# Kernel tuning notes

Measured on AMD Instinct MI355X. Metric: run time of the kernel, lower is better.

The kernel has to match this reference:

```python
import jax, jax.numpy as jnp
import numpy as np

B, S = 4, 1024
H = 32
NOPE, ROPE, VDIM = 128, 64, 128
Q_LORA, KV_LORA = 1536, 512
SCALE = 1.0 / np.sqrt(NOPE + ROPE)


def _make_rope(total, d, dtype=jnp.float32):
    # gen_rope: theta_j = 10000^{-2j/d}, idx = pos * theta, tiled x2 -> (T,1,d)
    theta = 1.0 / (10000.0 ** (jnp.arange(0, d, 2, dtype=dtype) / d))
    idx = jnp.arange(total, dtype=dtype)[:, None] * theta[None, :]  # (T, d/2)
    idx = jnp.tile(idx, (1, 2))[:, None, :]                          # (T, 1, d)
    return jnp.cos(idx), jnp.sin(idx)


def _apply_rope(x, cos, sin):
    # x: (T, heads, d); cos/sin: (T, 1, d). Matches torch apply_rope:
    # deinterleave even/odd then rotate-half.
    d = x.shape[-1]
    xp = jnp.concatenate([x[..., 0::2], x[..., 1::2]], axis=-1)
    rot = jnp.concatenate([-xp[..., d // 2:], xp[..., : d // 2]], axis=-1)
    return xp * cos + rot * sin


def setup_inputs() -> dict:
    key = jax.random.key(0)
    ks = jax.random.split(key, 5)
    Q = jax.random.normal(ks[0], (B, S, Q_LORA), dtype=jnp.float32)
    KV = jax.random.normal(ks[1], (B, S, KV_LORA), dtype=jnp.float32)
    PE = jax.random.normal(ks[2], (B, S, ROPE), dtype=jnp.float32)
    WUQ = jax.random.normal(ks[3], (H * (NOPE + ROPE), Q_LORA), dtype=jnp.float32) / np.sqrt(Q_LORA)
    WUKV = jax.random.normal(ks[4], (H * (NOPE + VDIM), KV_LORA), dtype=jnp.float32) / np.sqrt(KV_LORA)
    cos, sin = _make_rope(B * S, ROPE)
    return {"Q": Q, "KV": KV, "PE": PE, "WUQ": WUQ, "WUKV": WUKV, "cos": cos, "sin": sin}


def reference(Q, KV, PE, WUQ, WUKV, cos, sin):
    # Up-project Q latent -> per-head (nope + rope) dims
    q = jnp.einsum('bsl,el->bse', Q, WUQ).reshape(B, S, H, NOPE + ROPE)
    q_nope, q_pe = q[..., :NOPE], q[..., NOPE:]
    q_pe = _apply_rope(q_pe.reshape(B * S, H, ROPE), cos, sin).reshape(B, S, H, ROPE)
    # Shared (per-token) rotary key part
    k_pe = _apply_rope(PE.reshape(B * S, 1, ROPE), cos, sin).reshape(B, S, 1, ROPE)
    # Up-project KV latent -> per-head (k_nope + v)
    kvu = jnp.einsum('bsl,el->bse', KV, WUKV).reshape(B, S, H, NOPE + VDIM)
    k_nope, v = kvu[..., :NOPE], kvu[..., NOPE:]
    q_full = jnp.concatenate([q_nope, q_pe], axis=-1)                      # (B,S,H,192)
    k_full = jnp.concatenate([k_nope, jnp.broadcast_to(k_pe, (B, S, H, ROPE))], axis=-1)
    scores = jnp.einsum('bqhd,bkhd->bhqk', q_full, k_full) * SCALE        # (B,H,S,S)
    causal = jnp.tril(jnp.ones((S, S), dtype=bool))
    scores = jnp.where(causal, scores, jnp.finfo(scores.dtype).min)
    attn = jax.nn.softmax(scores, axis=-1)
    out = jnp.einsum('bhqk,bkhd->bqhd', attn, v)                          # (B,S,H,VDIM)
    return out
```

## Files before the change

kernel.cpp:

```cpp
#include <hip/hip_runtime.h>
#include <hip/hip_bf16.h>


typedef __attribute__((ext_vector_type(8))) short s8v;
typedef __attribute__((ext_vector_type(4))) short s4v;
typedef __attribute__((ext_vector_type(4))) float f4v;

#define B_ 4
#define S_ 1024
#define H_ 32
#define SCALE_ 0.07216878364870322992f

__device__ __forceinline__ short f2bf(float f) {
  unsigned u = __builtin_bit_cast(unsigned, f);
  unsigned r = (u + 0x7FFFu + ((u >> 16) & 1u)) >> 16;
  return (short)(unsigned short)r;
}

__device__ __forceinline__ void gll16(const void* g, void* l) {
  __builtin_amdgcn_global_load_lds((const __attribute__((address_space(1))) void*)g,
                                   (__attribute__((address_space(3))) void*)l, 16, 0, 0);
}

__global__ __launch_bounds__(256) void prep_kernel(
    const float* __restrict__ Q, const float* __restrict__ WUQ,
    const float* __restrict__ KV, const float* __restrict__ WUKV,
    const float* __restrict__ PE, const float* __restrict__ cosb,
    const float* __restrict__ sinb,
    short* __restrict__ Qb, short* __restrict__ Wq,
    short* __restrict__ KVb, short* __restrict__ Wkv,
    short* __restrict__ kfull) {
  const int b = blockIdx.x;
  if (b < 21504) {
    int i = b * 256 + threadIdx.x;
    const float* src; short* dst;
    if (i < 1572864)      { src = Q;    dst = Qb; }
    else if (i < 3932160) { src = WUQ;  dst = Wq;  i -= 1572864; }
    else if (i < 4456448) { src = KV;   dst = KVb; i -= 3932160; }
    else                  { src = WUKV; dst = Wkv; i -= 4456448; }
    float4 v = reinterpret_cast<const float4*>(src)[i];
    s4v o;
    o[0] = f2bf(v.x); o[1] = f2bf(v.y); o[2] = f2bf(v.z); o[3] = f2bf(v.w);
    reinterpret_cast<s4v*>(dst)[i] = o;
  } else {
    const int pos = (b - 21504) * 4 + (threadIdx.x >> 6);
    const int t = threadIdx.x & 63;
    const int p = t & 31;
    float x0 = PE[(size_t)pos * 64 + 2 * p];
    float x1 = PE[(size_t)pos * 64 + 2 * p + 1];
    float cv = cosb[(size_t)pos * 64 + p];
    float sv = sinb[(size_t)pos * 64 + p];
    float o = (t < 32) ? (x0 * cv - x1 * sv) : (x1 * cv + x0 * sv);
    short ob = f2bf(o);
    const int bb = pos >> 10, s = pos & 1023;
#pragma unroll
    for (int h = 0; h < H_; ++h)
      kfull[(((size_t)bb * H_ + h) * S_ + s) * 192 + 128 + t] = ob;
  }
}

template<int K, int MODE>
__device__ __forceinline__ void gemm_body(
    const int m0, const int n0, const short* __restrict__ A,
    const short* __restrict__ Bt, const float* __restrict__ cosb,
    const float* __restrict__ sinb, short* __restrict__ out0,
    short* __restrict__ out1, char* sAb, char* sBb) {
  const int tid = threadIdx.x;
  const int w = tid >> 6, l = tid & 63;
  const int l15 = l & 15, lg = l >> 4;
  const int wr = (w >> 1) * 64, wc = (w & 1) * 64;
  const int rs7 = l15 & 7;
  f4v acc[4][4] = {};
  const int srow = tid >> 3;
  const int swsl = (tid & 7) ^ (srow & 7);
  const char* gA = (const char*)A + ((size_t)(m0 + srow) * K + swsl * 8) * 2;
  const char* gB = (const char*)Bt + ((size_t)(n0 + srow) * K + swsl * 8) * 2;
  const int ldst = tid * 16;

#pragma unroll
  for (int r4 = 0; r4 < 4; ++r4) {
    gll16(gA + (size_t)r4 * (32 * K * 2), sAb + r4 * 4096 + ldst);
    gll16(gB + (size_t)r4 * (32 * K * 2), sBb + r4 * 4096 + ldst);
  }

  int cur = 0;
  for (int kk = 0; kk < K; kk += 64) {
    __syncthreads();
    if (kk + 64 < K) {
      const char* ga = gA + (size_t)(kk + 64) * 2;
      const char* gb = gB + (size_t)(kk + 64) * 2;
#pragma unroll
      for (int r4 = 0; r4 < 4; ++r4) {
        gll16(ga + (size_t)r4 * (32 * K * 2), sAb + (cur ^ 1) * 16384 + r4 * 4096 + ldst);
        gll16(gb + (size_t)r4 * (32 * K * 2), sBb + (cur ^ 1) * 16384 + r4 * 4096 + ldst);
      }
    }
#pragma unroll
    for (int kc = 0; kc < 2; ++kc) {
      s8v af[4], bfv[4];
#pragma unroll
      for (int x = 0; x < 4; ++x) {
        af[x]  = *(const s8v*)(sAb + cur * 16384 + (wr + x * 16 + l15) * 128 + (((kc * 4 + lg) ^ rs7) << 4));
        bfv[x] = *(const s8v*)(sBb + cur * 16384 + (wc + x * 16 + l15) * 128 + (((kc * 4 + lg) ^ rs7) << 4));
      }
#pragma unroll
      for (int i = 0; i < 4; ++i)
#pragma unroll
        for (int j = 0; j < 4; ++j)
          acc[i][j] = __builtin_amdgcn_mfma_f32_16x16x32_bf16(af[i], bfv[j], acc[i][j], 0, 0, 0);
    }
    cur ^= 1;
  }

#pragma unroll
  for (int j = 0; j < 4; ++j) {
    const int colb = n0 + wc + j * 16;
    if (MODE == 0) {
      const int e0 = colb % 192;
      const int h = colb / 192;
      const int e = e0 + l15;
      const bool is_pe = (e0 >= 128);
#pragma unroll
      for (int i = 0; i < 4; ++i) {
#pragma unroll
        for (int r = 0; r < 4; ++r) {
          const int row = m0 + wr + i * 16 + lg * 4 + r;
          const int b = row >> 10, s = row & 1023;
          const size_t base = ((size_t)(b * H_ + h) * S_ + s) * 192;
          float val = acc[i][j][r] * SCALE_;
          if (!is_pe) {
            out0[base + e] = f2bf(val);
          } else {
            float other = __shfl_xor(val, 1, 64);
            int p = (e - 128) >> 1;
            float cv = cosb[(size_t)row * 64 + p];
            float sv = sinb[(size_t)row * 64 + p];
            float o = ((l & 1) == 0) ? (val * cv - other * sv) : (val * cv + other * sv);
            int ep = ((l & 1) == 0) ? (128 + p) : (160 + p);
            out0[base + ep] = f2bf(o);
          }
        }
      }
    } else {
      const int e0 = colb % 256;
      const int h = colb / 256;
      const int e = e0 + l15;
      const bool is_v = (e0 >= 128);
#pragma unroll
      for (int i = 0; i < 4; ++i) {
#pragma unroll
        for (int r = 0; r < 4; ++r) {
          const int row = m0 + wr + i * 16 + lg * 4 + r;
          const int b = row >> 10, s = row & 1023;
          float val = acc[i][j][r];
          if (!is_v) {
            out0[((size_t)(b * H_ + h) * S_ + s) * 192 + e] = f2bf(val);
          } else {
            out1[((size_t)(b * H_ + h) * 128 + (e - 128)) * S_ + s] = f2bf(val);
          }
        }
      }
    }
  }
}

__global__ __launch_bounds__(256, 2) void gemm_fused(
    const short* __restrict__ Qb, const short* __restrict__ Wq,
    const short* __restrict__ KVb, const short* __restrict__ Wkv,
    const float* __restrict__ cosb, const float* __restrict__ sinb,
    short* __restrict__ qfull, short* __restrict__ kfull,
    short* __restrict__ vtb) {
  __shared__ char sAb[2 * 16384];
  __shared__ char sBb[2 * 16384];
  const int id = blockIdx.x;
  if (id < 1536) {
    const int xcd = id & 7, j = id >> 3;
    const int m0 = (xcd * 4 + (j & 3)) * 128;
    const int n0 = (j >> 2) * 128;
    gemm_body<1536, 0>(m0, n0, Qb, Wq, cosb, sinb, qfull, nullptr, sAb, sBb);
  } else {
    const int idp = id - 1536;
    const int xcd = idp & 7, j = idp >> 3;
    const int m0 = (xcd * 4 + (j & 3)) * 128;
    const int n0 = (j >> 2) * 128;
    gemm_body<512, 1>(m0, n0, KVb, Wkv, nullptr, nullptr, kfull, vtb, sAb, sBb);
  }
}

__global__ __launch_bounds__(256, 2) void attn_kernel(
    const short* __restrict__ qfull, const short* __restrict__ kfull,
    const short* __restrict__ vt, float* __restrict__ out) {
  __shared__ short sK[2][64 * 192];
  const int bid = blockIdx.x;
  const int qb = 7 - (bid >> 7);
  const int bh = bid & 127;
  const int b = bh >> 5, h = bh & 31;
  const int tid = threadIdx.x;
  const int w = tid >> 6, l = tid & 63;
  const int l15 = l & 15, lg = l >> 4;
  const short* Qh = qfull + (size_t)bh * (S_ * 192);
  const char*  KhB = (const char*)(kfull + (size_t)bh * (S_ * 192));
  const short* Vh = vt + (size_t)bh * (128 * S_);
  const int qw = qb * 128 + w * 32;

  s8v qfr[2][6];
#pragma unroll
  for (int mq = 0; mq < 2; ++mq)
#pragma unroll
    for (int kc = 0; kc < 6; ++kc)
      qfr[mq][kc] = *reinterpret_cast<const s8v*>(
          &Qh[(size_t)(qw + mq * 16 + l15) * 192 + kc * 32 + lg * 8]);

  unsigned kOff[6];
#pragma unroll
  for (int c = 0; c < 6; ++c) {
    unsigned o = (unsigned)(w * 6 + c) * 1024u + (unsigned)l * 16u;
    unsigned row = o / 384u;
    unsigned cb = o - row * 384u;
    kOff[c] = row * 384u + (cb ^ ((row & 7u) << 4));
  }

#pragma unroll
  for (int c = 0; c < 6; ++c)
    gll16(KhB + kOff[c], (char*)(&sK[0][0]) + (w * 6 + c) * 1024);
  __syncthreads();

  f4v acc[8][2] = {};
  float mrun[2] = {-3.0e38f, -3.0e38f};
  float lsum[2] = {0.f, 0.f};
  const int nt = 2 * (qb + 1);
  int cur = 0;
  for (int t = 0; t < nt; ++t) {
    const int k0 = t * 64;
    const bool compute = (k0 <= qw + 31);
    s8v vf0[8];
    if (compute) {
#pragma unroll
      for (int dt = 0; dt < 8; ++dt)
        vf0[dt] = *reinterpret_cast<const s8v*>(
            &Vh[(size_t)(dt * 16 + l15) * S_ + k0 + lg * 8]);
    }
    if (t + 1 < nt) {
      const char* gb = KhB + (size_t)(t + 1) * (64 * 384);
      char* lb = (char*)(&sK[cur ^ 1][0]);
#pragma unroll
      for (int c = 0; c < 6; ++c)
        gll16(gb + kOff[c], lb + (w * 6 + c) * 1024);
    }
    if (compute) {
      const char* sKc = (const char*)(&sK[cur][0]);
      f4v s[4][2] = {};
#pragma unroll
      for (int T = 0; T < 4; ++T) {
        const int row = T * 16 + l15;
        const unsigned swz = (unsigned)((row & 7) << 4);
#pragma unroll
        for (int kc = 0; kc < 6; ++kc) {
          s8v kf = *reinterpret_cast<const s8v*>(
              sKc + row * 384 + (unsigned)((kc * 64 + lg * 16) ^ swz));
          s[T][0] = __builtin_amdgcn_mfma_f32_16x16x32_bf16(kf, qfr[0][kc], s[T][0], 0, 0, 0);
          s[T][1] = __builtin_amdgcn_mfma_f32_16x16x32_bf16(kf, qfr[1][kc], s[T][1], 0, 0, 0);
        }
      }
      const bool diag = (t >= 2 * qb);
      unsigned pk[4][2][2];
#pragma unroll
      for (int mq = 0; mq < 2; ++mq) {
        const int qlane = qw + mq * 16 + l15;
        if (diag) {
#pragma unroll
          for (int T = 0; T < 4; ++T)
#pragma unroll
            for (int r = 0; r < 4; ++r)
              if (k0 + T * 16 + lg * 4 + r > qlane) s[T][mq][r] = -1.0e30f;
        }
        float tmax = s[0][mq][0];
#pragma unroll
        for (int T = 0; T < 4; ++T)
#pragma unroll
          for (int r = 0; r < 4; ++r) tmax = fmaxf(tmax, s[T][mq][r]);
        tmax = fmaxf(tmax, __shfl_xor(tmax, 16, 64));
        tmax = fmaxf(tmax, __shfl_xor(tmax, 32, 64));
        if (!__all(tmax <= mrun[mq] + 8.0f)) {
          const float mnew = fmaxf(mrun[mq], tmax);
          const float cf = __expf(mrun[mq] - mnew);
          mrun[mq] = mnew;
          lsum[mq] *= cf;
#pragma unroll
          for (int dt = 0; dt < 8; ++dt)
#pragma unroll
            for (int r = 0; r < 4; ++r) acc[dt][mq][r] *= cf;
        }
        float rs = 0.f;
#pragma unroll
        for (int T = 0; T < 4; ++T)
#pragma unroll
          for (int r = 0; r < 4; ++r) {
            float e = __expf(s[T][mq][r] - mrun[mq]);
            s[T][mq][r] = e;
            rs += e;
          }
        rs += __shfl_xor(rs, 16, 64);
        rs += __shfl_xor(rs, 32, 64);
        lsum[mq] += rs;
#pragma unroll
        for (int T = 0; T < 4; ++T) {
          pk[T][mq][0] = (unsigned)(unsigned short)f2bf(s[T][mq][0]) |
                         ((unsigned)(unsigned short)f2bf(s[T][mq][1]) << 16);
          pk[T][mq][1] = (unsigned)(unsigned short)f2bf(s[T][mq][2]) |
                         ((unsigned)(unsigned short)f2bf(s[T][mq][3]) << 16);
        }
      }
#pragma unroll
      for (int c2 = 0; c2 < 2; ++c2) {
        union { unsigned u[4]; s8v v; } bb[2];
#pragma unroll
        for (int mq = 0; mq < 2; ++mq)
#pragma unroll
          for (int j2 = 0; j2 < 4; ++j2) {
            int src = l15 + ((l & 16) << 1) + ((j2 & 2) << 3);
            unsigned va = (unsigned)__shfl((int)pk[2 * c2][mq][j2 & 1], src, 64);
            unsigned vb = (unsigned)__shfl((int)pk[2 * c2 + 1][mq][j2 & 1], src, 64);
            bb[mq].u[j2] = (l & 32) ? vb : va;
          }
#pragma unroll
        for (int dt = 0; dt < 8; ++dt) {
          s8v vfx = (c2 == 0) ? vf0[dt]
                              : *reinterpret_cast<const s8v*>(
                                    &Vh[(size_t)(dt * 16 + l15) * S_ + k0 + 32 + lg * 8]);
          acc[dt][0] = __builtin_amdgcn_mfma_f32_16x16x32_bf16(vfx, bb[0].v, acc[dt][0], 0, 0, 0);
          acc[dt][1] = __builtin_amdgcn_mfma_f32_16x16x32_bf16(vfx, bb[1].v, acc[dt][1], 0, 0, 0);
        }
      }
    }
    __syncthreads();
    cur ^= 1;
  }
#pragma unroll
  for (int mq = 0; mq < 2; ++mq) {
    const float inv = 1.0f / lsum[mq];
    const int q = qw + mq * 16 + l15;
    float* ob = out + (((size_t)b * S_ + q) * H_ + h) * 128 + lg * 4;
#pragma unroll
    for (int dt = 0; dt < 8; ++dt) {
      float4 o4 = { acc[dt][mq][0] * inv, acc[dt][mq][1] * inv,
                    acc[dt][mq][2] * inv, acc[dt][mq][3] * inv };
      *reinterpret_cast<float4*>(ob + dt * 16) = o4;
    }
  }
}

extern "C" void kernel_launch(void* const* d_in, const int* in_sizes, int n_in,
                              void* d_out, int out_size, void* d_ws, size_t ws_size,
                              hipStream_t stream) {
  const float* Q    = (const float*)d_in[0];
  const float* KV   = (const float*)d_in[1];
  const float* PE   = (const float*)d_in[2];
  const float* WUQ  = (const float*)d_in[3];
  const float* WUKV = (const float*)d_in[4];
  const float* cosb = (const float*)d_in[5];
  const float* sinb = (const float*)d_in[6];
  float* out = (float*)d_out;
  char* ws = (char*)d_ws;

  short* Qb    = (short*)(ws);
  short* Wq    = (short*)(ws + 12582912);
  short* KVb   = (short*)(ws + 31457280);
  short* Wkv   = (short*)(ws + 35651584);
  short* qfull = (short*)(ws + 44040192);
  short* kfull = (short*)(ws + 94371840);
  short* vtb   = (short*)(ws + 144703488);

  prep_kernel<<<22528, 256, 0, stream>>>(Q, WUQ, KV, WUKV, PE, cosb, sinb,
                                         Qb, Wq, KVb, Wkv, kfull);
  gemm_fused<<<3584, 256, 0, stream>>>(Qb, Wq, KVb, Wkv, cosb, sinb,
                                       qfull, kfull, vtb);
  attn_kernel<<<1024, 256, 0, stream>>>(qfull, kfull, vtb, out);
}
```

Before: 314.3 us.

## Enlarge GEMM tiles to 256x128 with 8 waves and triple-buffered LDS pipeline

Changes the fused up-projection GEMM from 128x128 tiles with 4 waves to 256x128 tiles with 8 waves and 512 threads, halving the grid. The previous double-buffered, sync-per-step loop becomes a three-stage global-to-LDS prefetch ring with explicit vmcnt waits and raw barriers. It also raises wave priority around the MFMA block and hoists B fragments out of the inner loop. The aim is to hide global load latency and improve operand reuse. The cost is a much larger LDS footprint (144KB), which likely allows only one block per CU despite the launch bound hint.

```diff
diff --git a/kernel.cpp b/kernel.cpp
--- a/kernel.cpp
+++ b/kernel.cpp
@@ -65,51 +65,67 @@
     const short* __restrict__ Bt, const float* __restrict__ cosb,
     const float* __restrict__ sinb, short* __restrict__ out0,
     short* __restrict__ out1, char* sAb, char* sBb) {
+  constexpr int NT = K / 64;
   const int tid = threadIdx.x;
   const int w = tid >> 6, l = tid & 63;
   const int l15 = l & 15, lg = l >> 4;
-  const int wr = (w >> 1) * 64, wc = (w & 1) * 64;
+  const int wr = (w >> 1) * 64;
+  const int wc = (w & 1) * 64;
   const int rs7 = l15 & 7;
   f4v acc[4][4] = {};
   const int srow = tid >> 3;
-  const int swsl = (tid & 7) ^ (srow & 7);
-  const char* gA = (const char*)A + ((size_t)(m0 + srow) * K + swsl * 8) * 2;
-  const char* gB = (const char*)Bt + ((size_t)(n0 + srow) * K + swsl * 8) * 2;
+  const int lslot = (tid & 7) ^ (srow & 7);
+  const char* gA = (const char*)A + ((size_t)(m0 + srow) * K + lslot * 8) * 2;
+  const char* gB = (const char*)Bt + ((size_t)(n0 + srow) * K + lslot * 8) * 2;
   const int ldst = tid * 16;
 
-#pragma unroll
-  for (int r4 = 0; r4 < 4; ++r4) {
-    gll16(gA + (size_t)r4 * (32 * K * 2), sAb + r4 * 4096 + ldst);
-    gll16(gB + (size_t)r4 * (32 * K * 2), sBb + r4 * 4096 + ldst);
-  }
-
-  int cur = 0;
-  for (int kk = 0; kk < K; kk += 64) {
-    __syncthreads();
-    if (kk + 64 < K) {
-      const char* ga = gA + (size_t)(kk + 64) * 2;
-      const char* gb = gB + (size_t)(kk + 64) * 2;
-#pragma unroll
-      for (int r4 = 0; r4 < 4; ++r4) {
-        gll16(ga + (size_t)r4 * (32 * K * 2), sAb + (cur ^ 1) * 16384 + r4 * 4096 + ldst);
-        gll16(gb + (size_t)r4 * (32 * K * 2), sBb + (cur ^ 1) * 16384 + r4 * 4096 + ldst);
-      }
-    }
-#pragma unroll
-    for (int kc = 0; kc < 2; ++kc) {
-      s8v af[4], bfv[4];
-#pragma unroll
-      for (int x = 0; x < 4; ++x) {
-        af[x]  = *(const s8v*)(sAb + cur * 16384 + (wr + x * 16 + l15) * 128 + (((kc * 4 + lg) ^ rs7) << 4));
-        bfv[x] = *(const s8v*)(sBb + cur * 16384 + (wc + x * 16 + l15) * 128 + (((kc * 4 + lg) ^ rs7) << 4));
-      }
-#pragma unroll
-      for (int i = 0; i < 4; ++i)
-#pragma unroll
-        for (int j = 0; j < 4; ++j)
-          acc[i][j] = __builtin_amdgcn_mfma_f32_16x16x32_bf16(af[i], bfv[j], acc[i][j], 0, 0, 0);
-    }
-    cur ^= 1;
+  auto stgA = [&](int buf, int kt) {
+#pragma unroll
+    for (int r4 = 0; r4 < 4; ++r4)
+      gll16(gA + (size_t)r4 * (64 * K * 2) + kt * 128, sAb + buf * 32768 + r4 * 8192 + ldst);
+  };
+  auto stgB = [&](int buf, int kt) {
+#pragma unroll
+    for (int r4 = 0; r4 < 2; ++r4)
+      gll16(gB + (size_t)r4 * (64 * K * 2) + kt * 128, sBb + buf * 16384 + r4 * 8192 + ldst);
+  };
+
+  stgA(0, 0); stgB(0, 0);
+  stgA(1, 1); stgB(1, 1);
+  asm volatile("s_waitcnt vmcnt(6)" ::: "memory");
+  __builtin_amdgcn_s_barrier();
+
+  int bi = 0;
+  for (int t = 0; t < NT; ++t) {
+    const char* bufA = sAb + bi * 32768;
+    const char* bufB = sBb + bi * 16384;
+    if (t + 2 < NT) {
+      int b2 = bi + 2; if (b2 >= 3) b2 -= 3;
+      stgA(b2, t + 2);
+      stgB(b2, t + 2);
+    }
+    s8v bf[2][4];
+#pragma unroll
+    for (int kc = 0; kc < 2; ++kc)
+#pragma unroll
+      for (int n = 0; n < 4; ++n)
+        bf[kc][n] = *(const s8v*)(bufB + (wc + n * 16 + l15) * 128 + (((kc * 4 + lg) ^ rs7) << 4));
+    __builtin_amdgcn_s_setprio(1);
+#pragma unroll
+    for (int kc = 0; kc < 2; ++kc)
+#pragma unroll
+      for (int i = 0; i < 4; ++i) {
+        s8v af = *(const s8v*)(bufA + (wr + i * 16 + l15) * 128 + (((kc * 4 + lg) ^ rs7) << 4));
+#pragma unroll
+        for (int n = 0; n < 4; ++n)
+          acc[i][n] = __builtin_amdgcn_mfma_f32_16x16x32_bf16(af, bf[kc][n], acc[i][n], 0, 0, 0);
+      }
+    __builtin_amdgcn_s_setprio(0);
+    if (t + 2 < NT) asm volatile("s_waitcnt vmcnt(6)" ::: "memory");
+    else            asm volatile("s_waitcnt vmcnt(0)" ::: "memory");
+    __builtin_amdgcn_sched_barrier(0);
+    __builtin_amdgcn_s_barrier();
+    bi = (bi == 2) ? 0 : bi + 1;
   }
 
 #pragma unroll
@@ -164,25 +180,25 @@
   }
 }
 
-__global__ __launch_bounds__(256, 2) void gemm_fused(
+__global__ __launch_bounds__(512, 2) void gemm_fused(
     const short* __restrict__ Qb, const short* __restrict__ Wq,
     const short* __restrict__ KVb, const short* __restrict__ Wkv,
     const float* __restrict__ cosb, const float* __restrict__ sinb,
     short* __restrict__ qfull, short* __restrict__ kfull,
     short* __restrict__ vtb) {
-  __shared__ char sAb[2 * 16384];
-  __shared__ char sBb[2 * 16384];
+  __shared__ char sAb[3 * 32768];
+  __shared__ char sBb[3 * 16384];
   const int id = blockIdx.x;
-  if (id < 1536) {
+  if (id < 768) {
     const int xcd = id & 7, j = id >> 3;
-    const int m0 = (xcd * 4 + (j & 3)) * 128;
-    const int n0 = (j >> 2) * 128;
+    const int m0 = (xcd * 2 + (j & 1)) * 256;
+    const int n0 = (j >> 1) * 128;
     gemm_body<1536, 0>(m0, n0, Qb, Wq, cosb, sinb, qfull, nullptr, sAb, sBb);
   } else {
-    const int idp = id - 1536;
+    const int idp = id - 768;
     const int xcd = idp & 7, j = idp >> 3;
-    const int m0 = (xcd * 4 + (j & 3)) * 128;
-    const int n0 = (j >> 2) * 128;
+    const int m0 = (xcd * 2 + (j & 1)) * 256;
+    const int n0 = (j >> 1) * 128;
     gemm_body<512, 1>(m0, n0, KVb, Wkv, nullptr, nullptr, kfull, vtb, sAb, sBb);
   }
 }
@@ -373,7 +389,7 @@
 
   prep_kernel<<<22528, 256, 0, stream>>>(Q, WUQ, KV, WUKV, PE, cosb, sinb,
                                          Qb, Wq, KVb, Wkv, kfull);
-  gemm_fused<<<3584, 256, 0, stream>>>(Qb, Wq, KVb, Wkv, cosb, sinb,
+  gemm_fused<<<1792, 512, 0, stream>>>(Qb, Wq, KVb, Wkv, cosb, sinb,
                                        qfull, kfull, vtb);
   attn_kernel<<<1024, 256, 0, stream>>>(qfull, kfull, vtb, out);
 }
```

After: 349.2 us. +11.1%, slower.
